# Performance work log

Measured on AMD Instinct MI355X. Metric: run time of the kernel, lower is better.

Reference implementation:

```python
import jax, jax.numpy as jnp
import numpy as np

N_NODES = 100000
N_EDGES = 1600000
IN_FEAT = 256
OUT_FEAT = 128


def setup_inputs() -> dict:
    key = jax.random.key(0)
    ks = jax.random.split(key, 8)
    x = jax.random.normal(ks[0], (N_NODES, IN_FEAT), dtype=jnp.float32)
    rows0 = jnp.sort(jax.random.randint(ks[1], (N_EDGES,), 0, N_NODES, dtype=jnp.int32))
    cols0 = jax.random.randint(ks[2], (N_EDGES,), 0, N_NODES, dtype=jnp.int32)
    vals0 = jax.random.uniform(ks[3], (N_EDGES,), dtype=jnp.float32)
    rows1 = jnp.sort(jax.random.randint(ks[4], (N_EDGES,), 0, N_NODES, dtype=jnp.int32))
    cols1 = jax.random.randint(ks[5], (N_EDGES,), 0, N_NODES, dtype=jnp.int32)
    vals1 = jax.random.uniform(ks[6], (N_EDGES,), dtype=jnp.float32)
    kw0, kw1 = jax.random.split(ks[7])
    # glorot-uniform-ish scale for [IN_FEAT, OUT_FEAT]
    limit = float(np.sqrt(6.0 / (IN_FEAT + OUT_FEAT)))
    W0 = jax.random.uniform(kw0, (IN_FEAT, OUT_FEAT), minval=-limit, maxval=limit, dtype=jnp.float32)
    W1 = jax.random.uniform(kw1, (IN_FEAT, OUT_FEAT), minval=-limit, maxval=limit, dtype=jnp.float32)
    return {"x": x, "rows0": rows0, "cols0": cols0, "vals0": vals0,
            "rows1": rows1, "cols1": cols1, "vals1": vals1, "W0": W0, "W1": W1}


def _spmm(rows, cols, vals, dense, n_rows):
    # sparse [N,N] (COO) @ dense [N,D] -> [N,D]
    gathered = vals[:, None] * dense[cols]          # [E, D]
    return jax.ops.segment_sum(gathered, rows, num_segments=n_rows)


def reference(x, rows0, cols0, vals0, rows1, cols1, vals1, W0, W1):
    # GraphConvolution with dropout=0 (identity), featureless=False, no bias, relu.
    # support_i = A_i @ (x @ W_i); output = relu(sum_i support_i)
    s0 = _spmm(rows0, cols0, vals0, x @ W0, N_NODES)
    s1 = _spmm(rows1, cols1, vals1, x @ W1, N_NODES)
    return jax.nn.relu(s0 + s1)
```

## Files before the change

### kernel.cpp

```cpp
#include <hip/hip_runtime.h>
#include <hip/hip_bf16.h>
#include <stdint.h>

#define NN   100000
#define NE   1600000
#define KIN  256
#define FOUT 128

typedef __attribute__((ext_vector_type(8))) short short8;
typedef __attribute__((ext_vector_type(4))) float f32x4;
typedef __attribute__((ext_vector_type(2))) float f32x2;

static __device__ __forceinline__ unsigned short f2bf(float f) {
  unsigned int u = __float_as_uint(f);
  u += 0x7fffu + ((u >> 16) & 1u);
  return (unsigned short)(u >> 16);
}

static __device__ __forceinline__ short8 pack8(float4 u, float4 v) {
  short8 r;
  r[0] = (short)f2bf(u.x); r[1] = (short)f2bf(u.y);
  r[2] = (short)f2bf(u.z); r[3] = (short)f2bf(u.w);
  r[4] = (short)f2bf(v.x); r[5] = (short)f2bf(v.y);
  r[6] = (short)f2bf(v.z); r[7] = (short)f2bf(v.w);
  return r;
}

__global__ void convert_w(const float* __restrict__ W0, const float* __restrict__ W1,
                          unsigned short* __restrict__ wt) {
  int n = blockIdx.x;
  int k = threadIdx.x;
  int which = blockIdx.y;
  const float* W = which ? W1 : W0;
  wt[(size_t)which * (FOUT * KIN) + n * KIN + k] = f2bf(W[k * FOUT + n]);
}

__global__ __launch_bounds__(256) void build_rowptr(const int* __restrict__ rows0,
                                                    const int* __restrict__ rows1,
                                                    int* __restrict__ rp0,
                                                    int* __restrict__ rp1) {
  const int e = blockIdx.x * 256 + threadIdx.x;
  const int* rows = blockIdx.y ? rows1 : rows0;
  int* rp = blockIdx.y ? rp1 : rp0;
  int r1 = rows[e];
  int r2 = (e + 1 < NE) ? rows[e + 1] : NN;
  if (e == 0)
    for (int r = 0; r <= r1; ++r) rp[r] = 0;
  for (int r = r1 + 1; r <= r2; ++r) rp[r] = e + 1;
}

__global__ __launch_bounds__(256) void gemm_fused(const float* __restrict__ x,
                                                  const unsigned short* __restrict__ wt,
                                                  unsigned short* __restrict__ h) {
  __shared__ __align__(16) unsigned short tile[4][2][16 * 128];

  const int tid  = threadIdx.x;
  const int lane = tid & 63;
  const int wv   = tid >> 6;
  const int m    = lane & 15;
  const int quad = lane >> 4;
  const int rowbase = blockIdx.x * 64 + wv * 16;

  int r  = rowbase + m;
  int rc = r < NN ? r : NN - 1;
  const float* ap = x + (size_t)rc * KIN + quad * 8;
  const unsigned short* bp = wt + (size_t)m * KIN + quad * 8;

  f32x4 acc0[8], acc1[8];
#pragma unroll
  for (int n = 0; n < 8; ++n) {
    acc0[n] = (f32x4){0.f, 0.f, 0.f, 0.f};
    acc1[n] = (f32x4){0.f, 0.f, 0.f, 0.f};
  }

#pragma unroll 2
  for (int ko = 0; ko < KIN; ko += 32) {
    float4 alo = *(const float4*)(ap + ko);
    float4 ahi = *(const float4*)(ap + ko + 4);
    short8 a = pack8(alo, ahi);
#pragma unroll
    for (int n = 0; n < 8; ++n) {
      short8 b0 = *(const short8*)(bp + (size_t)(n * 16) * KIN + ko);
      short8 b1 = *(const short8*)(bp + (size_t)(FOUT + n * 16) * KIN + ko);
      acc0[n] = __builtin_amdgcn_mfma_f32_16x16x32_bf16(a, b0, acc0[n], 0, 0, 0);
      acc1[n] = __builtin_amdgcn_mfma_f32_16x16x32_bf16(a, b1, acc1[n], 0, 0, 0);
    }
  }

#pragma unroll
  for (int n = 0; n < 8; ++n)
#pragma unroll
    for (int reg = 0; reg < 4; ++reg) {
      tile[wv][0][(quad * 4 + reg) * 128 + n * 16 + m] = f2bf(acc0[n][reg]);
      tile[wv][1][(quad * 4 + reg) * 128 + n * 16 + m] = f2bf(acc1[n][reg]);
    }

#pragma unroll
  for (int t = 0; t < 2; ++t) {
    unsigned short* hh = h + (size_t)t * NN * FOUT;
#pragma unroll
    for (int p = 0; p < 4; ++p) {
      int row  = p * 4 + quad;
      int colb = m * 8;
      uint4 v = *(const uint4*)&tile[wv][t][row * 128 + colb];
      int grow = rowbase + row;
      if (grow < NN)
        *(uint4*)&hh[(size_t)grow * FOUT + colb] = v;
    }
  }
}

static __device__ __forceinline__ void consume8(const float* __restrict__ vals, int i,
                                                const unsigned* g, float& sx, float& sy) {
#pragma unroll
  for (int u = 0; u < 8; ++u) {
    float v = vals[i + u];
    sx += v * __uint_as_float(g[u] << 16);
    sy += v * __uint_as_float(g[u] & 0xffff0000u);
  }
}

static __device__ __forceinline__ void tail_spmm(const int* __restrict__ cols,
                                                 const float* __restrict__ vals,
                                                 const unsigned short* __restrict__ hsrc,
                                                 int i, int e, int fo,
                                                 float& sx, float& sy) {
  for (; i + 4 <= e; i += 4) {
    int c0 = cols[i], c1 = cols[i + 1], c2 = cols[i + 2], c3 = cols[i + 3];
    unsigned g0 = *(const unsigned*)(hsrc + (size_t)c0 * FOUT + fo);
    unsigned g1 = *(const unsigned*)(hsrc + (size_t)c1 * FOUT + fo);
    unsigned g2 = *(const unsigned*)(hsrc + (size_t)c2 * FOUT + fo);
    unsigned g3 = *(const unsigned*)(hsrc + (size_t)c3 * FOUT + fo);
    float v0 = vals[i], v1 = vals[i + 1], v2 = vals[i + 2], v3 = vals[i + 3];
    sx += v0 * __uint_as_float(g0 << 16);
    sy += v0 * __uint_as_float(g0 & 0xffff0000u);
    sx += v1 * __uint_as_float(g1 << 16);
    sy += v1 * __uint_as_float(g1 & 0xffff0000u);
    sx += v2 * __uint_as_float(g2 << 16);
    sy += v2 * __uint_as_float(g2 & 0xffff0000u);
    sx += v3 * __uint_as_float(g3 << 16);
    sy += v3 * __uint_as_float(g3 & 0xffff0000u);
  }
  for (; i < e; ++i) {
    int c = cols[i];
    float v = vals[i];
    unsigned g = *(const unsigned*)(hsrc + (size_t)c * FOUT + fo);
    sx += v * __uint_as_float(g << 16);
    sy += v * __uint_as_float(g & 0xffff0000u);
  }
}

__global__ __launch_bounds__(256) void spmm_relu(
    const int* __restrict__ rp0, const int* __restrict__ cols0, const float* __restrict__ vals0,
    const int* __restrict__ rp1, const int* __restrict__ cols1, const float* __restrict__ vals1,
    const unsigned short* __restrict__ h, float* __restrict__ out) {
  const int lane = threadIdx.x & 63;
  int r = blockIdx.x * 4 + (threadIdx.x >> 6);
  r = __builtin_amdgcn_readfirstlane(r);
  const int fo = lane * 2;

  const unsigned short* h0 = h;
  const unsigned short* h1 = h + (size_t)NN * FOUT;

  int i0 = __builtin_amdgcn_readfirstlane(rp0[r]);
  int e0 = __builtin_amdgcn_readfirstlane(rp0[r + 1]);
  int i1 = __builtin_amdgcn_readfirstlane(rp1[r]);
  int e1 = __builtin_amdgcn_readfirstlane(rp1[r + 1]);

  float sx = 0.f, sy = 0.f;

  while (i0 + 8 <= e0 && i1 + 8 <= e1) {
    unsigned g0[8], g1[8];
#pragma unroll
    for (int u = 0; u < 8; ++u) {
      int c = cols0[i0 + u];
      g0[u] = *(const unsigned*)(h0 + (size_t)c * FOUT + fo);
    }
#pragma unroll
    for (int u = 0; u < 8; ++u) {
      int c = cols1[i1 + u];
      g1[u] = *(const unsigned*)(h1 + (size_t)c * FOUT + fo);
    }
    consume8(vals0, i0, g0, sx, sy);
    consume8(vals1, i1, g1, sx, sy);
    i0 += 8;
    i1 += 8;
  }
  tail_spmm(cols0, vals0, h0, i0, e0, fo, sx, sy);
  tail_spmm(cols1, vals1, h1, i1, e1, fo, sx, sy);

  f32x2 o;
  o.x = sx > 0.f ? sx : 0.f;
  o.y = sy > 0.f ? sy : 0.f;
  __builtin_nontemporal_store(o, (f32x2*)(out + (size_t)r * FOUT + fo));
}

extern "C" void kernel_launch(void* const* d_in, const int* in_sizes, int n_in,
                              void* d_out, int out_size, void* d_ws, size_t ws_size,
                              hipStream_t stream) {
  const float* x     = (const float*)d_in[0];
  const int*   rows0 = (const int*)d_in[1];
  const int*   cols0 = (const int*)d_in[2];
  const float* vals0 = (const float*)d_in[3];
  const int*   rows1 = (const int*)d_in[4];
  const int*   cols1 = (const int*)d_in[5];
  const float* vals1 = (const float*)d_in[6];
  const float* W0    = (const float*)d_in[7];
  const float* W1    = (const float*)d_in[8];
  float* out = (float*)d_out;

  char* ws = (char*)d_ws;
  unsigned short* wt = (unsigned short*)(ws);
  unsigned short* h  = (unsigned short*)(ws + 131072);
  int* rp0 = (int*)(ws + 51331072);
  int* rp1 = (int*)(ws + 51731136);

  build_rowptr<<<dim3(6250, 2), 256, 0, stream>>>(rows0, rows1, rp0, rp1);
  convert_w<<<dim3(128, 2), 256, 0, stream>>>(W0, W1, wt);
  gemm_fused<<<dim3((NN + 63) / 64, 1), 256, 0, stream>>>(x, wt, h);
  spmm_relu<<<25000, 256, 0, stream>>>(rp0, cols0, vals0, rp1, cols1, vals1, h, out);
}
```

Before: 410.7 us.

## Stage W tiles in swizzled LDS with double buffering, 32 rows per wave

The GEMM kernel now stages bf16 weight chunks in LDS through a double-buffered, XOR-swizzled layout instead of having every wave read B straight from global memory. Each wave now computes 32 rows rather than 16, so every B fragment feeds two MFMAs, and A loads are prefetched one k-step ahead. The aim is to cut redundant global and L2 traffic for W and raise MFMA utilisation. The cost is more registers and LDS (64 KB) per block, which may lower occupancy, and half as many blocks.

After: 350.2 us. -14.7%, faster.

```diff
diff --git a/kernel.cpp b/kernel.cpp
--- a/kernel.cpp
+++ b/kernel.cpp
@@ -52,60 +52,109 @@
 __global__ __launch_bounds__(256) void gemm_fused(const float* __restrict__ x,
                                                   const unsigned short* __restrict__ wt,
                                                   unsigned short* __restrict__ h) {
-  __shared__ __align__(16) unsigned short tile[4][2][16 * 128];
+  __shared__ __align__(16) unsigned short bbuf[2][2 * 128 * 64];
 
   const int tid  = threadIdx.x;
   const int lane = tid & 63;
   const int wv   = tid >> 6;
   const int m    = lane & 15;
   const int quad = lane >> 4;
-  const int rowbase = blockIdx.x * 64 + wv * 16;
-
-  int r  = rowbase + m;
-  int rc = r < NN ? r : NN - 1;
-  const float* ap = x + (size_t)rc * KIN + quad * 8;
-  const unsigned short* bp = wt + (size_t)m * KIN + quad * 8;
-
-  f32x4 acc0[8], acc1[8];
-#pragma unroll
-  for (int n = 0; n < 8; ++n) {
-    acc0[n] = (f32x4){0.f, 0.f, 0.f, 0.f};
-    acc1[n] = (f32x4){0.f, 0.f, 0.f, 0.f};
-  }
-
-#pragma unroll 2
-  for (int ko = 0; ko < KIN; ko += 32) {
-    float4 alo = *(const float4*)(ap + ko);
-    float4 ahi = *(const float4*)(ap + ko + 4);
-    short8 a = pack8(alo, ahi);
-#pragma unroll
-    for (int n = 0; n < 8; ++n) {
-      short8 b0 = *(const short8*)(bp + (size_t)(n * 16) * KIN + ko);
-      short8 b1 = *(const short8*)(bp + (size_t)(FOUT + n * 16) * KIN + ko);
-      acc0[n] = __builtin_amdgcn_mfma_f32_16x16x32_bf16(a, b0, acc0[n], 0, 0, 0);
-      acc1[n] = __builtin_amdgcn_mfma_f32_16x16x32_bf16(a, b1, acc1[n], 0, 0, 0);
-    }
-  }
-
-#pragma unroll
-  for (int n = 0; n < 8; ++n)
-#pragma unroll
-    for (int reg = 0; reg < 4; ++reg) {
-      tile[wv][0][(quad * 4 + reg) * 128 + n * 16 + m] = f2bf(acc0[n][reg]);
-      tile[wv][1][(quad * 4 + reg) * 128 + n * 16 + m] = f2bf(acc1[n][reg]);
-    }
-
+  const int rowbase = blockIdx.x * 128 + wv * 32;
+
+  int r0 = rowbase + m;
+  int r1 = rowbase + 16 + m;
+  int r0c = r0 < NN ? r0 : NN - 1;
+  int r1c = r1 < NN ? r1 : NN - 1;
+  const float* ap0 = x + (size_t)r0c * KIN + quad * 8;
+  const float* ap1 = x + (size_t)r1c * KIN + quad * 8;
+
+  f32x4 acc[2][2][8];
+#pragma unroll
+  for (int t = 0; t < 2; ++t)
+#pragma unroll
+    for (int i = 0; i < 2; ++i)
+#pragma unroll
+      for (int n = 0; n < 8; ++n)
+        acc[t][i][n] = (f32x4){0.f, 0.f, 0.f, 0.f};
+
+  uint4 sreg[8];
+#define STAGE_LOAD(ko_) do {                                                   \
+    _Pragma("unroll")                                                          \
+    for (int u = 0; u < 8; ++u) {                                              \
+      int pid = u * 256 + tid; int tm = pid >> 10;                             \
+      int c = (pid >> 3) & 127; int s = pid & 7;                               \
+      sreg[u] = *(const uint4*)(wt + (size_t)tm * (FOUT * KIN) + c * KIN +     \
+                                (ko_) + s * 8);                                \
+    } } while (0)
+#define STAGE_WRITE(buf_) do {                                                 \
+    _Pragma("unroll")                                                          \
+    for (int u = 0; u < 8; ++u) {                                              \
+      int pid = u * 256 + tid; int tm = pid >> 10;                             \
+      int c = (pid >> 3) & 127; int s = pid & 7;                               \
+      *(uint4*)&bbuf[buf_][tm * 8192 + c * 64 + ((s ^ (c & 7)) * 8)] = sreg[u];\
+    } } while (0)
+
+  float4 fc[4], fn[4];
+  fc[0] = *(const float4*)(ap0);     fc[1] = *(const float4*)(ap0 + 4);
+  fc[2] = *(const float4*)(ap1);     fc[3] = *(const float4*)(ap1 + 4);
+
+  STAGE_LOAD(0);
+  STAGE_WRITE(0);
+  __syncthreads();
+
+#pragma unroll
+  for (int ci = 0; ci < 4; ++ci) {
+    if (ci < 3) STAGE_LOAD((ci + 1) * 64);
+#pragma unroll
+    for (int kk = 0; kk < 2; ++kk) {
+      const int ki = ci * 2 + kk;
+      if (ki < 7) {
+        const int off = (ki + 1) * 32;
+        fn[0] = *(const float4*)(ap0 + off);     fn[1] = *(const float4*)(ap0 + off + 4);
+        fn[2] = *(const float4*)(ap1 + off);     fn[3] = *(const float4*)(ap1 + off + 4);
+      }
+      short8 a0 = pack8(fc[0], fc[1]);
+      short8 a1 = pack8(fc[2], fc[3]);
+      const unsigned short* bb = &bbuf[ci & 1][0];
+#pragma unroll
+      for (int t = 0; t < 2; ++t)
+#pragma unroll
+        for (int n = 0; n < 8; ++n) {
+          const int col = n * 16 + m;
+          short8 b = *(const short8*)(bb + t * 8192 + col * 64 +
+                                      (((kk * 4 + quad) ^ (m & 7)) * 8));
+          acc[t][0][n] = __builtin_amdgcn_mfma_f32_16x16x32_bf16(a0, b, acc[t][0][n], 0, 0, 0);
+          acc[t][1][n] = __builtin_amdgcn_mfma_f32_16x16x32_bf16(a1, b, acc[t][1][n], 0, 0, 0);
+        }
+      fc[0] = fn[0]; fc[1] = fn[1]; fc[2] = fn[2]; fc[3] = fn[3];
+    }
+    if (ci < 3) {
+      STAGE_WRITE((ci + 1) & 1);
+      __syncthreads();
+    }
+  }
+#undef STAGE_LOAD
+#undef STAGE_WRITE
+
+  unsigned short* tile = &bbuf[0][0] + wv * 4096;
 #pragma unroll
   for (int t = 0; t < 2; ++t) {
+#pragma unroll
+    for (int i = 0; i < 2; ++i)
+#pragma unroll
+      for (int n = 0; n < 8; ++n)
+#pragma unroll
+        for (int reg = 0; reg < 4; ++reg)
+          tile[(i * 16 + quad * 4 + reg) * 128 + n * 16 + m] = f2bf(acc[t][i][n][reg]);
+
     unsigned short* hh = h + (size_t)t * NN * FOUT;
 #pragma unroll
-    for (int p = 0; p < 4; ++p) {
-      int row  = p * 4 + quad;
-      int colb = m * 8;
-      uint4 v = *(const uint4*)&tile[wv][t][row * 128 + colb];
+    for (int p = 0; p < 8; ++p) {
+      int row = p * 4 + quad;
+      uint4 v = *(const uint4*)&tile[row * 128 + m * 8];
       int grow = rowbase + row;
       if (grow < NN)
-        *(uint4*)&hh[(size_t)grow * FOUT + colb] = v;
+        *(uint4*)&hh[(size_t)grow * FOUT + m * 8] = v;
     }
   }
 }
@@ -217,6 +266,6 @@
 
   build_rowptr<<<dim3(6250, 2), 256, 0, stream>>>(rows0, rows1, rp0, rp1);
   convert_w<<<dim3(128, 2), 256, 0, stream>>>(W0, W1, wt);
-  gemm_fused<<<dim3((NN + 63) / 64, 1), 256, 0, stream>>>(x, wt, h);
+  gemm_fused<<<dim3((NN + 127) / 128, 1), 256, 0, stream>>>(x, wt, h);
   spmm_relu<<<25000, 256, 0, stream>>>(rp0, cols0, vals0, rp1, cols1, vals1, h, out);
 }
```

## Stage W tiles in LDS via async global_load_lds with double buffering

Applied to the files above, without the earlier changes.

The GEMM kernel now loads bf16 weight chunks into shared memory with direct global-to-LDS DMA, using a double buffer and an XOR swizzle. Previously every wave read its B fragments straight from global memory. Blocks grow to 512 threads covering 128 rows, so each staged chunk is reused by eight waves, and the next x fragment is prefetched into registers. The output tile reuses the B buffer, which adds block-wide syncs and LDS traffic in exchange for less redundant global/L2 reading of W.

New measurement: 332.2 us (median of 2 runs). 1.24x faster.

```diff
diff --git a/kernel.cpp b/kernel.cpp
--- a/kernel.cpp
+++ b/kernel.cpp
@@ -49,63 +49,94 @@
   for (int r = r1 + 1; r <= r2; ++r) rp[r] = e + 1;
 }
 
-__global__ __launch_bounds__(256) void gemm_fused(const float* __restrict__ x,
-                                                  const unsigned short* __restrict__ wt,
-                                                  unsigned short* __restrict__ h) {
-  __shared__ __align__(16) unsigned short tile[4][2][16 * 128];
+__global__ __launch_bounds__(512, 4) void gemm_fused(const float* __restrict__ x,
+                                                     const unsigned short* __restrict__ wt,
+                                                     unsigned short* __restrict__ h) {
+  __shared__ __align__(16) unsigned short bbuf[2][2 * 128 * 64];
 
   const int tid  = threadIdx.x;
   const int lane = tid & 63;
   const int wv   = tid >> 6;
   const int m    = lane & 15;
   const int quad = lane >> 4;
-  const int rowbase = blockIdx.x * 64 + wv * 16;
+  const int rowbase = blockIdx.x * 128 + wv * 16;
 
   int r  = rowbase + m;
   int rc = r < NN ? r : NN - 1;
   const float* ap = x + (size_t)rc * KIN + quad * 8;
-  const unsigned short* bp = wt + (size_t)m * KIN + quad * 8;
-
-  f32x4 acc0[8], acc1[8];
-#pragma unroll
-  for (int n = 0; n < 8; ++n) {
-    acc0[n] = (f32x4){0.f, 0.f, 0.f, 0.f};
-    acc1[n] = (f32x4){0.f, 0.f, 0.f, 0.f};
-  }
-
-#pragma unroll 2
-  for (int ko = 0; ko < KIN; ko += 32) {
-    float4 alo = *(const float4*)(ap + ko);
-    float4 ahi = *(const float4*)(ap + ko + 4);
-    short8 a = pack8(alo, ahi);
-#pragma unroll
-    for (int n = 0; n < 8; ++n) {
-      short8 b0 = *(const short8*)(bp + (size_t)(n * 16) * KIN + ko);
-      short8 b1 = *(const short8*)(bp + (size_t)(FOUT + n * 16) * KIN + ko);
-      acc0[n] = __builtin_amdgcn_mfma_f32_16x16x32_bf16(a, b0, acc0[n], 0, 0, 0);
-      acc1[n] = __builtin_amdgcn_mfma_f32_16x16x32_bf16(a, b1, acc1[n], 0, 0, 0);
-    }
-  }
-
-#pragma unroll
-  for (int n = 0; n < 8; ++n)
-#pragma unroll
-    for (int reg = 0; reg < 4; ++reg) {
-      tile[wv][0][(quad * 4 + reg) * 128 + n * 16 + m] = f2bf(acc0[n][reg]);
-      tile[wv][1][(quad * 4 + reg) * 128 + n * 16 + m] = f2bf(acc1[n][reg]);
-    }
-
+
+  f32x4 acc[2][8];
+#pragma unroll
+  for (int t = 0; t < 2; ++t)
+#pragma unroll
+    for (int n = 0; n < 8; ++n)
+      acc[t][n] = (f32x4){0.f, 0.f, 0.f, 0.f};
+
+#define STAGE_DMA(ko_, buf_) do {                                              \
+    _Pragma("unroll")                                                          \
+    for (int u = 0; u < 4; ++u) {                                              \
+      int pid = u * 512 + tid;                                                 \
+      int tm = pid >> 10; int c = (pid >> 3) & 127; int s = pid & 7;           \
+      const unsigned short* g = wt + (size_t)tm * (FOUT * KIN) + c * KIN +     \
+                                (ko_) + ((s ^ (c & 7)) * 8);                   \
+      __builtin_amdgcn_global_load_lds(                                        \
+          (const __attribute__((address_space(1))) void*)g,                    \
+          (__attribute__((address_space(3))) void*)                            \
+              &bbuf[buf_][(size_t)(u * 512 + wv * 64) * 8],                    \
+          16, 0, 0);                                                           \
+    } } while (0)
+
+  float4 fc0 = *(const float4*)(ap);
+  float4 fc1 = *(const float4*)(ap + 4);
+
+  STAGE_DMA(0, 0);
+  __syncthreads();
+
+#pragma unroll
+  for (int ci = 0; ci < 4; ++ci) {
+    if (ci < 3) STAGE_DMA((ci + 1) * 64, (ci + 1) & 1);
+#pragma unroll
+    for (int kk = 0; kk < 2; ++kk) {
+      const int ki = ci * 2 + kk;
+      float4 fn0, fn1;
+      if (ki < 7) {
+        fn0 = *(const float4*)(ap + (ki + 1) * 32);
+        fn1 = *(const float4*)(ap + (ki + 1) * 32 + 4);
+      }
+      short8 a = pack8(fc0, fc1);
+      const unsigned short* bb = &bbuf[ci & 1][0];
+#pragma unroll
+      for (int t = 0; t < 2; ++t)
+#pragma unroll
+        for (int n = 0; n < 8; ++n) {
+          const int col = n * 16 + m;
+          short8 b = *(const short8*)(bb + t * 8192 + col * 64 +
+                                      (((kk * 4 + quad) ^ (m & 7)) * 8));
+          acc[t][n] = __builtin_amdgcn_mfma_f32_16x16x32_bf16(a, b, acc[t][n], 0, 0, 0);
+        }
+      fc0 = fn0; fc1 = fn1;
+    }
+    if (ci < 3) __syncthreads();
+  }
+#undef STAGE_DMA
+
+  unsigned short* tile = &bbuf[0][0] + wv * 2048;
 #pragma unroll
   for (int t = 0; t < 2; ++t) {
+#pragma unroll
+    for (int n = 0; n < 8; ++n)
+#pragma unroll
+      for (int reg = 0; reg < 4; ++reg)
+        tile[(quad * 4 + reg) * 128 + n * 16 + m] = f2bf(acc[t][n][reg]);
+
     unsigned short* hh = h + (size_t)t * NN * FOUT;
 #pragma unroll
     for (int p = 0; p < 4; ++p) {
-      int row  = p * 4 + quad;
-      int colb = m * 8;
-      uint4 v = *(const uint4*)&tile[wv][t][row * 128 + colb];
+      int row = p * 4 + quad;
+      uint4 v = *(const uint4*)&tile[row * 128 + m * 8];
       int grow = rowbase + row;
       if (grow < NN)
-        *(uint4*)&hh[(size_t)grow * FOUT + colb] = v;
+        *(uint4*)&hh[(size_t)grow * FOUT + m * 8] = v;
     }
   }
 }
@@ -217,6 +248,6 @@
 
   build_rowptr<<<dim3(6250, 2), 256, 0, stream>>>(rows0, rows1, rp0, rp1);
   convert_w<<<dim3(128, 2), 256, 0, stream>>>(W0, W1, wt);
-  gemm_fused<<<dim3((NN + 63) / 64, 1), 256, 0, stream>>>(x, wt, h);
+  gemm_fused<<<dim3((NN + 127) / 128, 1), 512, 0, stream>>>(x, wt, h);
   spmm_relu<<<25000, 256, 0, stream>>>(rp0, cols0, vals0, rp1, cols1, vals1, h, out);
 }
```
